# Kernel tuning notes

Hardware: AMD Instinct MI355X
Metric: run time of the kernel (lower is better)

The kernel has to match this reference:

```python
import jax, jax.numpy as jnp
import numpy as np

INF = 1.0e6  # sentinel distance for rows/cols with no background pixel


def _edt(mask):
    """Exact 2D Euclidean distance transform.

    For each pixel of mask [B,C,H,W], returns the Euclidean distance to the
    nearest pixel where mask == 0 (scipy.ndimage.distance_transform_edt
    semantics: nonzero = foreground, zero = background/feature).
    Uses the separable 2-pass algorithm: 1D distance along H, then an exact
    min over parabolas along W (done as a vectorized scan over column index).
    """
    B, C, H, W = mask.shape
    is_fg = mask != 0  # [B,C,H,W]

    # ---- pass 1: 1D distance along axis H to nearest zero in same column ----
    fg_h = jnp.moveaxis(is_fg, 2, 0)  # [H,B,C,W]

    def run_step(d, fg_row):  # d: [B,C,W]
        d = jnp.where(fg_row, d + 1.0, 0.0)
        return d, d

    init = jnp.full((B, C, W), INF, jnp.float32)
    _, d_fwd = jax.lax.scan(run_step, init, fg_h)
    _, d_bwd = jax.lax.scan(run_step, init, fg_h, reverse=True)
    g = jnp.minimum(jnp.minimum(d_fwd, d_bwd), INF)  # [H,B,C,W]
    f = jnp.moveaxis(g * g, 0, 2)  # [B,C,H,W] squared vertical distance

    # ---- pass 2: D[...,j] = min_k (j-k)^2 + f[...,k]  (exact 2D sq. EDT) ----
    js = jnp.arange(W, dtype=jnp.float32)  # [W]
    f_k = jnp.moveaxis(f, 3, 0)  # [W,B,C,H]

    def min_step(D, xs):
        k, fk = xs  # scalar, [B,C,H]
        cand = (js - k) ** 2 + fk[..., None]  # [B,C,H,W]
        return jnp.minimum(D, cand), None

    D0 = jnp.full((B, C, H, W), INF * INF, jnp.float32)
    D, _ = jax.lax.scan(min_step, D0, (js, f_k))
    return jnp.sqrt(D)


def setup_inputs() -> dict:
    key = jax.random.key(0)
    k1, k2 = jax.random.split(key)
    B, C, H, W = 16, 1, 512, 512
    output = jax.random.normal(k1, (B, C, H, W), dtype=jnp.float32)
    target = jax.random.randint(k2, (B, C, H, W), 0, 2, dtype=jnp.int32)
    return {"output": output, "target": target}


def reference(output, target):
    prob = jax.nn.sigmoid(output)  # [B,C,H,W]
    tgt = target.astype(jnp.float32)
    # signed distance: distance inside foreground minus distance inside background
    dist = _edt(1.0 - tgt) - _edt(tgt)  # [B,C,H,W]
    return jnp.mean(prob * dist)
```

## Files before the change

### kernel.cpp

```cpp
#include <hip/hip_runtime.h>
#include <math.h>

#define HDIM 512
#define WDIM 512
#define SEG 16
#define SROWS 32
#define VCOLS 32
#define VTHREADS 512
#define ROWS_PB 4
#define HTHREADS 256
#define PAD 32
#define LROW (WDIM + 2 * PAD)
#define INF_I (1 << 20)
#define ENC_SENT 127
#define P1RAD 4
#define P1BOUND 25.0f


__global__ __launch_bounds__(VTHREADS) void vert_pass9(const int* __restrict__ tgt,
                                                       signed char* __restrict__ sdist) {
    __shared__ int s_fs1[SEG][VCOLS], s_ls1[SEG][VCOLS];
    __shared__ int s_fs0[SEG][VCOLS], s_ls0[SEG][VCOLS];
    __shared__ int s_c1f[SEG][VCOLS], s_c1b[SEG][VCOLS];
    __shared__ int s_c0f[SEG][VCOLS], s_c0b[SEG][VCOLS];

    int tid = threadIdx.x;
    int w = tid & (VCOLS - 1);
    int seg = tid >> 5;
    int bW = WDIM / VCOLS;
    int b = blockIdx.x / bW;
    int wbase = (blockIdx.x % bW) * VCOLS;
    size_t colbase = (size_t)b * HDIM * WDIM + wbase + w;
    const int* col = tgt + colbase + (size_t)(seg * SROWS) * WDIM;

    unsigned R1 = 0u;
    #pragma unroll 8
    for (int h = 0; h < SROWS; ++h) {
        int tv = col[(size_t)h * WDIM];
        R1 |= ((unsigned)(tv != 0)) << h;
    }
    unsigned R0 = ~R1;

    s_fs1[seg][w] = R1 ? __builtin_ctz(R1) : SROWS;
    s_ls1[seg][w] = R1 ? 31 - __builtin_clz(R1) : -1;
    s_fs0[seg][w] = R0 ? __builtin_ctz(R0) : SROWS;
    s_ls0[seg][w] = R0 ? 31 - __builtin_clz(R0) : -1;
    __syncthreads();

    if (tid < 128) {
        int cw = tid & (VCOLS - 1);
        int md = tid >> 5;
        int c = INF_I;
        if (md == 0) {
            for (int s = 0; s < SEG; ++s) {
                s_c1f[s][cw] = c;
                int ls = s_ls1[s][cw];
                c = (ls >= 0) ? (SROWS - 1 - ls) : c + SROWS;
            }
        } else if (md == 1) {
            for (int s = SEG - 1; s >= 0; --s) {
                s_c1b[s][cw] = c;
                int fs = s_fs1[s][cw];
                c = (fs < SROWS) ? fs : c + SROWS;
            }
        } else if (md == 2) {
            for (int s = 0; s < SEG; ++s) {
                s_c0f[s][cw] = c;
                int ls = s_ls0[s][cw];
                c = (ls >= 0) ? (SROWS - 1 - ls) : c + SROWS;
            }
        } else {
            for (int s = SEG - 1; s >= 0; --s) {
                s_c0b[s][cw] = c;
                int fs = s_fs0[s][cw];
                c = (fs < SROWS) ? fs : c + SROWS;
            }
        }
    }
    __syncthreads();

    int c1f = s_c1f[seg][w], c1b = s_c1b[seg][w];
    int c0f = s_c0f[seg][w], c0b = s_c0b[seg][w];

    signed char* os = sdist + colbase + (size_t)(seg * SROWS) * WDIM;

    unsigned mle = 0u;
    for (int h = 0; h < SROWS; ++h) {
        mle = (mle << 1) | 1u;
        unsigned a1 = R1 & mle;
        int d1f = a1 ? (h - (31 - __builtin_clz(a1))) : c1f + h + 1;
        unsigned b1 = R1 >> h;
        int d1b = b1 ? __builtin_ctz(b1) : c1b + (SROWS - h);
        int g1 = min(d1f, d1b);
        unsigned a0 = R0 & mle;
        int d0f = a0 ? (h - (31 - __builtin_clz(a0))) : c0f + h + 1;
        unsigned b0 = R0 >> h;
        int d0b = b0 ? __builtin_ctz(b0) : c0b + (SROWS - h);
        int g0 = min(d0f, d0b);

        signed char sval = ((R1 >> h) & 1u) ? (signed char)(-min(g0, ENC_SENT))
                                            : (signed char)min(g1, ENC_SENT);
        os[(size_t)h * WDIM] = sval;
    }
}

__global__ __launch_bounds__(HTHREADS) void horiz_pass9(const int* __restrict__ sdist4,
                                                        const float* __restrict__ outp,
                                                        double* __restrict__ partial) {
    __shared__ float sf1[ROWS_PB * LROW];
    __shared__ float sf0[ROWS_PB * LROW];
    __shared__ unsigned short wl[ROWS_PB * WDIM];
    __shared__ int wcnt;
    __shared__ double swave[4];

    int tid = threadIdx.x;
    size_t base = (size_t)blockIdx.x * (ROWS_PB * WDIM);

    if (tid == 0) wcnt = 0;
    if (tid < ROWS_PB * 2 * PAD) {
        int r = tid / (2 * PAD);
        int c = tid % (2 * PAD);
        int off = r * LROW + (c < PAD ? c : WDIM + c);
        sf1[off] = 3.0e12f;
        sf0[off] = 3.0e12f;
    }

    const int* sp = sdist4 + base / 4;
    for (int i = tid; i < (ROWS_PB * WDIM) / 4; i += HTHREADS) {
        int p = sp[i];
        int j = i * 4;
        int row = j >> 9;
        int lbase = row * LROW + PAD + (j & (WDIM - 1));
        #pragma unroll
        for (int k = 0; k < 4; ++k) {
            int sv = (p << (24 - 8 * k)) >> 24;
            int neg = sv < 0;
            int e = neg ? -sv : sv;
            float g = (e >= ENC_SENT) ? 1.0e6f : (float)e;
            float f = g * g;
            sf1[lbase + k] = neg ? 0.0f : f;
            sf0[lbase + k] = neg ? f : 0.0f;
        }
    }
    __syncthreads();

    double local = 0.0;

    #pragma unroll
    for (int g = 0; g < 2; ++g) {
        int idx0 = (g * HTHREADS + tid) * 4;
        int row = idx0 >> 9;
        int j0 = idx0 & (WDIM - 1);
        float4 xq = *(const float4*)(outp + base + idx0);
        float xs[4] = {xq.x, xq.y, xq.z, xq.w};
        const float* e1 = sf1 + row * LROW + PAD;
        const float* e0 = sf0 + row * LROW + PAD;
        #pragma unroll
        for (int q = 0; q < 4; ++q) {
            int j = j0 + q;
            bool cls0 = e1[j] > 0.0f;
            const float* env = cls0 ? e1 : e0;
            float best = env[j];
            #pragma unroll
            for (int rad = 1; rad <= P1RAD; ++rad) {
                float rr = (float)(rad * rad);
                best = fminf(best, fminf(rr + env[j - rad], rr + env[j + rad]));
            }
            if (best <= P1BOUND) {
                float sd = sqrtf(best);
                float dist = cls0 ? sd : -sd;
                float prob = 1.0f / (1.0f + expf(-xs[q]));
                local += (double)(prob * dist);
            } else {
                int slot = atomicAdd(&wcnt, 1);
                wl[slot] = (unsigned short)(idx0 + q);
            }
        }
    }
    __syncthreads();

    int cnt = wcnt;
    for (int i = tid; i < cnt; i += HTHREADS) {
        int id = wl[i];
        int row = id >> 9;
        int j = id & (WDIM - 1);
        const float* e1 = sf1 + row * LROW + PAD;
        const float* e0 = sf0 + row * LROW + PAD;
        bool cls0 = e1[j] > 0.0f;
        const float* env = cls0 ? e1 : e0;
        float best = env[j];
        #pragma unroll
        for (int rad = 1; rad <= P1RAD; ++rad) {
            float rr = (float)(rad * rad);
            best = fminf(best, fminf(rr + env[j - rad], rr + env[j + rad]));
        }
        float rr = (float)((P1RAD + 1) * (P1RAD + 1));
        for (int rad = P1RAD + 1; rad <= PAD; ++rad) {
            if (rr >= best) break;
            best = fminf(best, fminf(rr + env[j - rad], rr + env[j + rad]));
            rr += 2.0f * (float)rad + 1.0f;
        }
        if (best > (float)((PAD + 1) * (PAD + 1))) {
            for (int rad = PAD + 1; rad < WDIM; ++rad) {
                float r2 = (float)(rad * rad);
                if (r2 >= best) break;
                int kl = j - rad; kl = kl < 0 ? 0 : kl;
                int kr = j + rad; kr = kr > WDIM - 1 ? WDIM - 1 : kr;
                best = fminf(best, fminf(r2 + env[kl], r2 + env[kr]));
            }
        }
        float sd = sqrtf(best);
        float dist = cls0 ? sd : -sd;
        float x = outp[base + id];
        float prob = 1.0f / (1.0f + expf(-x));
        local += (double)(prob * dist);
    }

    double v = local;
    #pragma unroll
    for (int off = 32; off > 0; off >>= 1) v += __shfl_down(v, off, 64);
    int wid = tid >> 6, lane = tid & 63;
    if (lane == 0) swave[wid] = v;
    __syncthreads();
    if (tid == 0) partial[blockIdx.x] = swave[0] + swave[1] + swave[2] + swave[3];
}

__global__ __launch_bounds__(256) void finalize9(const double* __restrict__ partial,
                                                 float* __restrict__ out,
                                                 int npart, double invN) {
    __shared__ double swave[4];
    int tid = threadIdx.x;
    double local = 0.0;
    for (int i = tid; i < npart; i += 256) local += partial[i];
    #pragma unroll
    for (int off = 32; off > 0; off >>= 1) local += __shfl_down(local, off, 64);
    int wid = tid >> 6, lane = tid & 63;
    if (lane == 0) swave[wid] = local;
    __syncthreads();
    if (tid == 0) out[0] = (float)((swave[0] + swave[1] + swave[2] + swave[3]) * invN);
}

extern "C" void kernel_launch(void* const* d_in, const int* in_sizes, int n_in,
                              void* d_out, int out_size, void* d_ws, size_t ws_size,
                              hipStream_t stream) {
    const float* outp = (const float*)d_in[0];
    const int* tgt = (const int*)d_in[1];
    int N = in_sizes[0];
    int B = N / (HDIM * WDIM);

    int npart = (B * HDIM) / ROWS_PB;

    double* partial = (double*)((char*)d_ws + 256);
    signed char* sdist = (signed char*)((char*)d_ws + 32768);

    vert_pass9<<<B * (WDIM / VCOLS), VTHREADS, 0, stream>>>(tgt, sdist);
    horiz_pass9<<<npart, HTHREADS, 0, stream>>>((const int*)sdist, outp, partial);
    finalize9<<<1, 256, 0, stream>>>(partial, (float*)d_out, npart, 1.0 / (double)N);
}
```

Measured before the change: 30.67 us.

## Register-window horizontal EDT search and drop shared-memory worklist

In the horizontal pass, each thread now loads a 16-float window of both envelopes from LDS into registers with float4 loads and evaluates radii 1-4 from registers. When any of its four pixels exceeds the radius-4 bound, it extends to radii 5-8 with one more float4 load and then scans the rest serially. This replaces the shared atomic worklist and the second phase, and it also vectorizes the envelope stores and halves the padding. The aim is fewer scalar LDS reads and atomics, at the cost of more registers and divergent tails inside a warp.

```diff
diff --git a/kernel.cpp b/kernel.cpp
--- a/kernel.cpp
+++ b/kernel.cpp
@@ -9,16 +9,14 @@
 #define VTHREADS 512
 #define ROWS_PB 4
 #define HTHREADS 256
-#define PAD 32
+#define PAD 16
 #define LROW (WDIM + 2 * PAD)
 #define INF_I (1 << 20)
 #define ENC_SENT 127
-#define P1RAD 4
-#define P1BOUND 25.0f
-
-
-__global__ __launch_bounds__(VTHREADS) void vert_pass9(const int* __restrict__ tgt,
-                                                       signed char* __restrict__ sdist) {
+
+
+__global__ __launch_bounds__(VTHREADS) void vert_pass10(const int* __restrict__ tgt,
+                                                        signed char* __restrict__ sdist) {
     __shared__ int s_fs1[SEG][VCOLS], s_ls1[SEG][VCOLS];
     __shared__ int s_fs0[SEG][VCOLS], s_ls0[SEG][VCOLS];
     __shared__ int s_c1f[SEG][VCOLS], s_c1b[SEG][VCOLS];
@@ -104,19 +102,16 @@
     }
 }
 
-__global__ __launch_bounds__(HTHREADS) void horiz_pass9(const int* __restrict__ sdist4,
-                                                        const float* __restrict__ outp,
-                                                        double* __restrict__ partial) {
+__global__ __launch_bounds__(HTHREADS) void horiz_pass10(const int* __restrict__ sdist4,
+                                                         const float* __restrict__ outp,
+                                                         double* __restrict__ partial) {
     __shared__ float sf1[ROWS_PB * LROW];
     __shared__ float sf0[ROWS_PB * LROW];
-    __shared__ unsigned short wl[ROWS_PB * WDIM];
-    __shared__ int wcnt;
     __shared__ double swave[4];
 
     int tid = threadIdx.x;
     size_t base = (size_t)blockIdx.x * (ROWS_PB * WDIM);
 
-    if (tid == 0) wcnt = 0;
     if (tid < ROWS_PB * 2 * PAD) {
         int r = tid / (2 * PAD);
         int c = tid % (2 * PAD);
@@ -131,6 +126,9 @@
         int j = i * 4;
         int row = j >> 9;
         int lbase = row * LROW + PAD + (j & (WDIM - 1));
+        float4 q1, q0;
+        float* q1f = (float*)&q1;
+        float* q0f = (float*)&q0;
         #pragma unroll
         for (int k = 0; k < 4; ++k) {
             int sv = (p << (24 - 8 * k)) >> 24;
@@ -138,9 +136,11 @@
             int e = neg ? -sv : sv;
             float g = (e >= ENC_SENT) ? 1.0e6f : (float)e;
             float f = g * g;
-            sf1[lbase + k] = neg ? 0.0f : f;
-            sf0[lbase + k] = neg ? f : 0.0f;
-        }
+            q1f[k] = neg ? 0.0f : f;
+            q0f[k] = neg ? f : 0.0f;
+        }
+        *(float4*)(sf1 + lbase) = q1;
+        *(float4*)(sf0 + lbase) = q0;
     }
     __syncthreads();
 
@@ -151,69 +151,84 @@
         int idx0 = (g * HTHREADS + tid) * 4;
         int row = idx0 >> 9;
         int j0 = idx0 & (WDIM - 1);
+        int wb = row * LROW + PAD + j0;
         float4 xq = *(const float4*)(outp + base + idx0);
-        float xs[4] = {xq.x, xq.y, xq.z, xq.w};
-        const float* e1 = sf1 + row * LROW + PAD;
-        const float* e0 = sf0 + row * LROW + PAD;
+
+        float w1[16], w0[16];
+        *(float4*)(w1 + 0)  = *(const float4*)(sf1 + wb - 8);
+        *(float4*)(w1 + 4)  = *(const float4*)(sf1 + wb - 4);
+        *(float4*)(w1 + 8)  = *(const float4*)(sf1 + wb + 0);
+        *(float4*)(w1 + 12) = *(const float4*)(sf1 + wb + 4);
+        *(float4*)(w0 + 0)  = *(const float4*)(sf0 + wb - 8);
+        *(float4*)(w0 + 4)  = *(const float4*)(sf0 + wb - 4);
+        *(float4*)(w0 + 8)  = *(const float4*)(sf0 + wb + 0);
+        *(float4*)(w0 + 12) = *(const float4*)(sf0 + wb + 4);
+
+        float best[4];
+        bool cls[4];
         #pragma unroll
         for (int q = 0; q < 4; ++q) {
-            int j = j0 + q;
-            bool cls0 = e1[j] > 0.0f;
-            const float* env = cls0 ? e1 : e0;
-            float best = env[j];
+            bool c0 = w1[8 + q] > 0.0f;
+            cls[q] = c0;
+            float b = c0 ? w1[8 + q] : w0[8 + q];
             #pragma unroll
-            for (int rad = 1; rad <= P1RAD; ++rad) {
+            for (int rad = 1; rad <= 4; ++rad) {
                 float rr = (float)(rad * rad);
-                best = fminf(best, fminf(rr + env[j - rad], rr + env[j + rad]));
-            }
-            if (best <= P1BOUND) {
-                float sd = sqrtf(best);
-                float dist = cls0 ? sd : -sd;
-                float prob = 1.0f / (1.0f + expf(-xs[q]));
-                local += (double)(prob * dist);
-            } else {
-                int slot = atomicAdd(&wcnt, 1);
-                wl[slot] = (unsigned short)(idx0 + q);
-            }
-        }
-    }
-    __syncthreads();
-
-    int cnt = wcnt;
-    for (int i = tid; i < cnt; i += HTHREADS) {
-        int id = wl[i];
-        int row = id >> 9;
-        int j = id & (WDIM - 1);
-        const float* e1 = sf1 + row * LROW + PAD;
-        const float* e0 = sf0 + row * LROW + PAD;
-        bool cls0 = e1[j] > 0.0f;
-        const float* env = cls0 ? e1 : e0;
-        float best = env[j];
+                float cl = c0 ? w1[8 + q - rad] : w0[8 + q - rad];
+                float cr = c0 ? w1[8 + q + rad] : w0[8 + q + rad];
+                b = fminf(b, fminf(rr + cl, rr + cr));
+            }
+            best[q] = b;
+        }
+
+        float qmax = fmaxf(fmaxf(best[0], best[1]), fmaxf(best[2], best[3]));
+        if (qmax > 25.0f) {
+            float e1[4], e0[4];
+            *(float4*)e1 = *(const float4*)(sf1 + wb + 8);
+            *(float4*)e0 = *(const float4*)(sf0 + wb + 8);
+            #pragma unroll
+            for (int q = 0; q < 4; ++q) {
+                bool c0 = cls[q];
+                float b = best[q];
+                #pragma unroll
+                for (int rad = 5; rad <= 8; ++rad) {
+                    float rr = (float)(rad * rad);
+                    int li = 8 + q - rad;
+                    int ri = 8 + q + rad;
+                    float cl = c0 ? w1[li] : w0[li];
+                    float cr = (ri < 16) ? (c0 ? w1[ri] : w0[ri])
+                                         : (c0 ? e1[ri - 16] : e0[ri - 16]);
+                    b = fminf(b, fminf(rr + cl, rr + cr));
+                }
+                best[q] = b;
+            }
+            #pragma unroll
+            for (int q = 0; q < 4; ++q) {
+                if (best[q] > 81.0f) {
+                    int j = j0 + q;
+                    const float* env = (cls[q] ? sf1 : sf0) + row * LROW + PAD;
+                    float b = best[q];
+                    float rr = 81.0f;
+                    for (int rad = 9; rad < WDIM; ++rad) {
+                        if (rr >= b) break;
+                        int kl = j - rad; kl = kl < 0 ? 0 : kl;
+                        int kr = j + rad; kr = kr > WDIM - 1 ? WDIM - 1 : kr;
+                        b = fminf(b, fminf(rr + env[kl], rr + env[kr]));
+                        rr += 2.0f * (float)rad + 1.0f;
+                    }
+                    best[q] = b;
+                }
+            }
+        }
+
+        const float* xs = (const float*)&xq;
         #pragma unroll
-        for (int rad = 1; rad <= P1RAD; ++rad) {
-            float rr = (float)(rad * rad);
-            best = fminf(best, fminf(rr + env[j - rad], rr + env[j + rad]));
-        }
-        float rr = (float)((P1RAD + 1) * (P1RAD + 1));
-        for (int rad = P1RAD + 1; rad <= PAD; ++rad) {
-            if (rr >= best) break;
-            best = fminf(best, fminf(rr + env[j - rad], rr + env[j + rad]));
-            rr += 2.0f * (float)rad + 1.0f;
-        }
-        if (best > (float)((PAD + 1) * (PAD + 1))) {
-            for (int rad = PAD + 1; rad < WDIM; ++rad) {
-                float r2 = (float)(rad * rad);
-                if (r2 >= best) break;
-                int kl = j - rad; kl = kl < 0 ? 0 : kl;
-                int kr = j + rad; kr = kr > WDIM - 1 ? WDIM - 1 : kr;
-                best = fminf(best, fminf(r2 + env[kl], r2 + env[kr]));
-            }
-        }
-        float sd = sqrtf(best);
-        float dist = cls0 ? sd : -sd;
-        float x = outp[base + id];
-        float prob = 1.0f / (1.0f + expf(-x));
-        local += (double)(prob * dist);
+        for (int q = 0; q < 4; ++q) {
+            float sd = sqrtf(best[q]);
+            float dist = cls[q] ? sd : -sd;
+            float prob = 1.0f / (1.0f + expf(-xs[q]));
+            local += (double)(prob * dist);
+        }
     }
 
     double v = local;
@@ -225,9 +240,9 @@
     if (tid == 0) partial[blockIdx.x] = swave[0] + swave[1] + swave[2] + swave[3];
 }
 
-__global__ __launch_bounds__(256) void finalize9(const double* __restrict__ partial,
-                                                 float* __restrict__ out,
-                                                 int npart, double invN) {
+__global__ __launch_bounds__(256) void finalize10(const double* __restrict__ partial,
+                                                  float* __restrict__ out,
+                                                  int npart, double invN) {
     __shared__ double swave[4];
     int tid = threadIdx.x;
     double local = 0.0;
@@ -253,7 +268,7 @@
     double* partial = (double*)((char*)d_ws + 256);
     signed char* sdist = (signed char*)((char*)d_ws + 32768);
 
-    vert_pass9<<<B * (WDIM / VCOLS), VTHREADS, 0, stream>>>(tgt, sdist);
-    horiz_pass9<<<npart, HTHREADS, 0, stream>>>((const int*)sdist, outp, partial);
-    finalize9<<<1, 256, 0, stream>>>(partial, (float*)d_out, npart, 1.0 / (double)N);
-}
+    vert_pass10<<<B * (WDIM / VCOLS), VTHREADS, 0, stream>>>(tgt, sdist);
+    horiz_pass10<<<npart, HTHREADS, 0, stream>>>((const int*)sdist, outp, partial);
+    finalize10<<<1, 256, 0, stream>>>(partial, (float*)d_out, npart, 1.0 / (double)N);
+}
```

Result: faster. 28.36 us (-7.5%).
